# Kernel tuning notes

Hardware: AMD Instinct MI355X
Metric: run time of the kernel (lower is better)

## Reference

```python
import jax, jax.numpy as jnp
import numpy as np

K = 4

def grid_sample_bilinear_zeros(img, grid):
    # img: [b,c,H,W]; grid: [b,h,w,2] normalized coords (x,y) in [-1,1]
    # PyTorch grid_sample, mode='bilinear', padding_mode='zeros', align_corners=False
    b, c, H, W = img.shape
    h, w = grid.shape[1], grid.shape[2]
    ix = (grid[..., 0] + 1.0) * (W * 0.5) - 0.5
    iy = (grid[..., 1] + 1.0) * (H * 0.5) - 0.5
    x0 = jnp.floor(ix); y0 = jnp.floor(iy)
    wx1 = ix - x0; wx0 = 1.0 - wx1
    wy1 = iy - y0; wy0 = 1.0 - wy1
    x0i = x0.astype(jnp.int32); y0i = y0.astype(jnp.int32)
    x1i = x0i + 1; y1i = y0i + 1
    imgf = img.reshape(b, c, H * W)
    N = h * w

    def gather(xi, yi, wgt):
        valid = (xi >= 0) & (xi < W) & (yi >= 0) & (yi < H)
        xc = jnp.clip(xi, 0, W - 1); yc = jnp.clip(yi, 0, H - 1)
        idx = (yc * W + xc).reshape(b, 1, N)
        g = jnp.take_along_axis(imgf, jnp.broadcast_to(idx, (b, c, N)), axis=2)
        wv = (wgt * valid.astype(img.dtype)).reshape(b, 1, N)
        return g * wv

    out = (gather(x0i, y0i, wx0 * wy0) + gather(x1i, y0i, wx1 * wy0) +
           gather(x0i, y1i, wx0 * wy1) + gather(x1i, y1i, wx1 * wy1))
    return out.reshape(b, c, h, w)


def setup_inputs() -> dict:
    key = jax.random.key(0)
    ks = jax.random.split(key, 8)
    b, c, h, w = 8, 256, 96, 96
    out_ch = 256
    x = jax.random.normal(ks[0], (b, c, h, w), dtype=jnp.float32)
    Wc = jax.random.normal(ks[1], (out_ch, c), dtype=jnp.float32) * 0.02
    bc = jax.random.normal(ks[2], (out_ch,), dtype=jnp.float32) * 0.02
    Woff = jax.random.normal(ks[3], (K, 2, c), dtype=jnp.float32) * 0.02
    boff = jax.random.normal(ks[4], (K, 2), dtype=jnp.float32) * 0.02
    Wwt = jax.random.normal(ks[5], (K, c), dtype=jnp.float32) * 0.02
    bwt = jax.random.normal(ks[6], (K,), dtype=jnp.float32) * 0.02
    return {"x": x, "Wc": Wc, "bc": bc, "Woff": Woff, "boff": boff, "Wwt": Wwt, "bwt": bwt}


def reference(x, Wc, bc, Woff, boff, Wwt, bwt):
    b, c, h, w = x.shape
    # 1x1 conv projection
    proj = jnp.einsum('bchw,oc->bohw', x, Wc) + bc[None, :, None, None]
    # k flow fields, each [b,2,h,w] -> [k,b,h,w,2]
    flows = jnp.einsum('bchw,koc->kbohw', x, Woff) + boff[:, None, :, None, None]
    flows = jnp.transpose(flows, (0, 1, 3, 4, 2))
    # softmax sampling weights [b,k,h,w]
    logits = jnp.einsum('bchw,kc->bkhw', x, Wwt) + bwt[None, :, None, None]
    weights = jax.nn.softmax(logits, axis=1)
    # base pixel grid (x,y)
    gy, gx = jnp.meshgrid(jnp.arange(h, dtype=x.dtype), jnp.arange(w, dtype=x.dtype), indexing='ij')
    base = jnp.stack((gx, gy), axis=-1)  # [h,w,2]
    vgrid = base[None, None] + flows  # [k,b,h,w,2]
    vx = 2.0 * vgrid[..., 0] / max(w - 1, 1) - 1.0
    vy = 2.0 * vgrid[..., 1] / max(h - 1, 1) - 1.0
    vgrid_scaled = jnp.stack((vx, vy), axis=-1)  # [k,b,h,w,2]
    feats = jax.vmap(lambda g: grid_sample_bilinear_zeros(proj, g))(vgrid_scaled)  # [k,b,o,h,w]
    out = jnp.einsum('kbohw,bkhw->bohw', feats, weights)
    return out
```

## Files before the change

kernel.cpp:

```cpp
#include <hip/hip_runtime.h>

#define HW   9216
#define IMG  96
#define NB   8
#define NK   4

typedef __bf16 bf16x8 __attribute__((ext_vector_type(8)));
typedef float  f32x4  __attribute__((ext_vector_type(4)));

__device__ __forceinline__ unsigned short f2bf(float f) {
    unsigned int u = __float_as_uint(f);
    u += 0x7FFFu + ((u >> 16) & 1u);
    return (unsigned short)(u >> 16);
}

extern "C" __global__ __launch_bounds__(256, 4)
void prep_kernel(const float* __restrict__ x,
                 const float* __restrict__ Wc,
                 const float* __restrict__ Woff,
                 const float* __restrict__ boff,
                 const float* __restrict__ Wwt,
                 const float* __restrict__ bwt,
                 unsigned short* __restrict__ xbt,
                 unsigned short* __restrict__ Wcb,
                 float2* __restrict__ coords,
                 float* __restrict__ wts)
{
    __shared__ __align__(16) unsigned short tile[64 * 266];

    const int t   = threadIdx.x;
    const int bxr = blockIdx.x;

    if (bxr >= NB * 144) {
        int u = ((bxr - NB * 144) * 256 + t) * 4;
        float4 v = *(const float4*)(Wc + u);
        union { unsigned short h[4]; int2 p; } pk;
        pk.h[0] = f2bf(v.x); pk.h[1] = f2bf(v.y);
        pk.h[2] = f2bf(v.z); pk.h[3] = f2bf(v.w);
        *(int2*)(Wcb + u) = pk.p;
        return;
    }

    const int b  = bxr / 144;
    const int p0 = (bxr % 144) * 64;
    const int px = t & 63;
    const int g  = __builtin_amdgcn_readfirstlane(t >> 6);

    float acc[12];
    #pragma unroll
    for (int j = 0; j < 12; ++j) acc[j] = 0.f;

    const float* xb = x + ((size_t)(b * 256 + g * 64)) * HW + p0 + px;
    unsigned int* trow = (unsigned int*)tile;

    for (int i0 = 0; i0 < 64; i0 += 8) {
        float v[8];
        #pragma unroll
        for (int q = 0; q < 8; ++q)
            v[q] = xb[(size_t)(i0 + q) * HW];
        #pragma unroll
        for (int q = 0; q < 8; ++q) {
            const int c = g * 64 + i0 + q;
            #pragma unroll
            for (int j = 0; j < 8; ++j) acc[j] += v[q] * Woff[j * 256 + c];
            #pragma unroll
            for (int j = 0; j < 4; ++j) acc[8 + j] += v[q] * Wwt[j * 256 + c];
        }
        #pragma unroll
        for (int q = 0; q < 8; q += 2) {
            unsigned int pk = (unsigned int)f2bf(v[q]) | ((unsigned int)f2bf(v[q + 1]) << 16);
            trow[px * 133 + ((g * 64 + i0 + q) >> 1)] = pk;
        }
    }

    __syncthreads();
    #pragma unroll
    for (int r = 0; r < 8; ++r) {
        int u = t + 256 * r;
        int sub = u & 31, p2 = u >> 5;
        int4 v = *(const int4*)(tile + p2 * 266 + sub * 8);
        *(int4*)(xbt + ((size_t)b * HW + p0 + p2) * 256 + sub * 8) = v;
    }
    __syncthreads();

    float* red = (float*)tile;
    #pragma unroll
    for (int j = 0; j < 12; ++j)
        red[(g * 64 + px) * 12 + j] = acc[j];
    __syncthreads();

    if (t < 64) {
        float s[12];
        #pragma unroll
        for (int j = 0; j < 12; ++j)
            s[j] = red[(0 * 64 + px) * 12 + j] + red[(1 * 64 + px) * 12 + j] +
                   red[(2 * 64 + px) * 12 + j] + red[(3 * 64 + px) * 12 + j];

        const int p = p0 + px;
        const float pyf = (float)(p / IMG);
        const float pxf = (float)(p % IMG);

        #pragma unroll
        for (int k = 0; k < NK; ++k) {
            float fx = s[k * 2 + 0] + boff[k * 2 + 0];
            float fy = s[k * 2 + 1] + boff[k * 2 + 1];
            float vx = 2.0f * (pxf + fx) / 95.0f - 1.0f;
            float vy = 2.0f * (pyf + fy) / 95.0f - 1.0f;
            float ix = (vx + 1.0f) * 48.0f - 0.5f;
            float iy = (vy + 1.0f) * 48.0f - 0.5f;
            coords[((size_t)k * NB + b) * HW + p] = make_float2(ix, iy);
        }
        float l0 = s[8] + bwt[0], l1 = s[9] + bwt[1];
        float l2 = s[10] + bwt[2], l3 = s[11] + bwt[3];
        float m = fmaxf(fmaxf(l0, l1), fmaxf(l2, l3));
        float e0 = __expf(l0 - m), e1 = __expf(l1 - m);
        float e2 = __expf(l2 - m), e3 = __expf(l3 - m);
        float inv = 1.0f / (e0 + e1 + e2 + e3);
        wts[((size_t)0 * NB + b) * HW + p] = e0 * inv;
        wts[((size_t)1 * NB + b) * HW + p] = e1 * inv;
        wts[((size_t)2 * NB + b) * HW + p] = e2 * inv;
        wts[((size_t)3 * NB + b) * HW + p] = e3 * inv;
    }
}

extern "C" __global__ __launch_bounds__(256, 3)
void fused_kernel(const unsigned short* __restrict__ Wcb,
                  const unsigned short* __restrict__ xbt,
                  const float2* __restrict__ coords,
                  const float* __restrict__ wts,
                  const float* __restrict__ bc,
                  float* __restrict__ out)
{
    __shared__ __align__(16) unsigned char lds[49408];
    unsigned short* BsU   = (unsigned short*)lds;
    unsigned short* AsU   = (unsigned short*)(lds + 32768);
    float*          cw    = (float*)(lds + 32768);
    unsigned int*   ci    = (unsigned int*)(lds + 36864);
    float*          wsumL = (float*)(lds + 49152);

    const int t  = threadIdx.x;
    const int bx = blockIdx.x;
    const int b  = bx & 7;
    const int p0 = (bx >> 3) * 64;

    {
        const int px = t & 63;
        const int k  = t >> 6;
        const int p  = p0 + px;
        float2 cc = coords[((size_t)k * NB + b) * HW + p];
        float wk  = wts[((size_t)k * NB + b) * HW + p];
        float x0f = floorf(cc.x), y0f = floorf(cc.y);
        float wx1 = cc.x - x0f, wx0 = 1.0f - wx1;
        float wy1 = cc.y - y0f, wy0 = 1.0f - wy1;
        int x0 = (int)x0f, y0 = (int)y0f;
        int x1 = x0 + 1,   y1 = y0 + 1;
        float vx0 = (x0 >= 0 && x0 < IMG) ? 1.f : 0.f;
        float vx1 = (x1 >= 0 && x1 < IMG) ? 1.f : 0.f;
        float vy0 = (y0 >= 0 && y0 < IMG) ? 1.f : 0.f;
        float vy1 = (y1 >= 0 && y1 < IMG) ? 1.f : 0.f;
        int cx0 = min(max(x0, 0), IMG - 1), cx1 = min(max(x1, 0), IMG - 1);
        int cy0 = min(max(y0, 0), IMG - 1), cy1 = min(max(y1, 0), IMG - 1);
        int i0 = cy0 * IMG + cx0, i1 = cy0 * IMG + cx1;
        int i2 = cy1 * IMG + cx0, i3 = cy1 * IMG + cx1;
        float w0 = wk * wx0 * wy0 * vx0 * vy0;
        float w1 = wk * wx1 * wy0 * vx1 * vy0;
        float w2 = wk * wx0 * wy1 * vx0 * vy1;
        float w3 = wk * wx1 * wy1 * vx1 * vy1;
        *(float4*)(cw + px * 16 + k * 4) = make_float4(w0, w1, w2, w3);
        uint2 ip;
        ip.x = (unsigned int)i0 | ((unsigned int)i1 << 16);
        ip.y = (unsigned int)i2 | ((unsigned int)i3 << 16);
        *(uint2*)(ci + px * 8 + k * 2) = ip;
    }
    __syncthreads();

    {
        if (t < 64) {
            float s = 0.f;
            #pragma unroll
            for (int j = 0; j < 16; ++j) s += cw[t * 16 + j];
            wsumL[t] = s;
        }
        const int pxl = t >> 5, ch = t & 31;
        const unsigned short* gbase = xbt + (size_t)b * HW * 256 + ch * 8;
        #pragma unroll 2
        for (int rep = 0; rep < 8; ++rep) {
            const int px = rep * 8 + pxl;
            float wl[16];
            #pragma unroll
            for (int q = 0; q < 4; ++q) {
                float4 wv = *(const float4*)(cw + px * 16 + q * 4);
                wl[q * 4 + 0] = wv.x; wl[q * 4 + 1] = wv.y;
                wl[q * 4 + 2] = wv.z; wl[q * 4 + 3] = wv.w;
            }
            unsigned int ip[8];
            #pragma unroll
            for (int q = 0; q < 2; ++q) {
                uint4 iv = *(const uint4*)(ci + px * 8 + q * 4);
                ip[q * 4 + 0] = iv.x; ip[q * 4 + 1] = iv.y;
                ip[q * 4 + 2] = iv.z; ip[q * 4 + 3] = iv.w;
            }
            int4 v[16];
            #pragma unroll
            for (int j = 0; j < 16; ++j) {
                unsigned int idx = (ip[j >> 1] >> ((j & 1) * 16)) & 0xFFFFu;
                v[j] = *(const int4*)(gbase + (size_t)idx * 256);
            }
            float acc[8];
            #pragma unroll
            for (int i = 0; i < 8; ++i) acc[i] = 0.f;
            #pragma unroll
            for (int j = 0; j < 16; ++j) {
                const unsigned int* u = (const unsigned int*)&v[j];
                float wj = wl[j];
                #pragma unroll
                for (int q = 0; q < 4; ++q) {
                    float lo = __uint_as_float(u[q] << 16);
                    float hi = __uint_as_float(u[q] & 0xFFFF0000u);
                    acc[2 * q + 0] += wj * lo;
                    acc[2 * q + 1] += wj * hi;
                }
            }
            union { unsigned short h[8]; int4 v4; } pk;
            #pragma unroll
            for (int i = 0; i < 8; ++i) pk.h[i] = f2bf(acc[i]);
            const int pos = ch ^ (px & 7);
            *(int4*)(BsU + px * 256 + pos * 8) = pk.v4;
        }
    }
    __syncthreads();

    const int lane = t & 63, wave = t >> 6;
    const int wm = wave * 64;
    const int l15 = lane & 15, quad = lane >> 4;

    f32x4 acc[4][4];
    #pragma unroll
    for (int mt = 0; mt < 4; ++mt)
        #pragma unroll
        for (int nt = 0; nt < 4; ++nt)
            acc[mt][nt] = (f32x4){0.f, 0.f, 0.f, 0.f};

    for (int k0 = 0; k0 < 256; k0 += 32) {
        #pragma unroll
        for (int i = 0; i < 4; ++i) {
            int u = t + 256 * i;
            int row = u >> 2, sub = u & 3;
            int sub_g = sub ^ ((row >> 1) & 3);
            __builtin_amdgcn_global_load_lds(
                (const __attribute__((address_space(1))) void*)(Wcb + (size_t)row * 256 + k0 + sub_g * 8),
                (__attribute__((address_space(3))) void*)(AsU + u * 8), 16, 0, 0);
        }
        __syncthreads();
        bf16x8 af[4], bf[4];
        #pragma unroll
        for (int mt = 0; mt < 4; ++mt) {
            int row = wm + mt * 16 + l15;
            int pos = quad ^ ((row >> 1) & 3);
            af[mt] = *(const bf16x8*)(const void*)(AsU + row * 32 + pos * 8);
        }
        #pragma unroll
        for (int nt = 0; nt < 4; ++nt) {
            int row = nt * 16 + l15;
            int pos = ((k0 >> 3) + quad) ^ (row & 7);
            bf[nt] = *(const bf16x8*)(const void*)(BsU + row * 256 + pos * 8);
        }
        #pragma unroll
        for (int mt = 0; mt < 4; ++mt)
            #pragma unroll
            for (int nt = 0; nt < 4; ++nt)
                acc[mt][nt] = __builtin_amdgcn_mfma_f32_16x16x32_bf16(af[mt], bf[nt], acc[mt][nt], 0, 0, 0);
        __syncthreads();
    }

    float wv[4];
    #pragma unroll
    for (int nt = 0; nt < 4; ++nt)
        wv[nt] = wsumL[nt * 16 + l15];

    #pragma unroll
    for (int mt = 0; mt < 4; ++mt) {
        int ob = wm + mt * 16 + quad * 4;
        #pragma unroll
        for (int reg = 0; reg < 4; ++reg) {
            int o = ob + reg;
            float bias = bc[o];
            float* dst = out + ((size_t)b * 256 + o) * HW + p0 + l15;
            #pragma unroll
            for (int nt = 0; nt < 4; ++nt)
                dst[nt * 16] = acc[mt][nt][reg] + bias * wv[nt];
        }
    }
}

extern "C" void kernel_launch(void* const* d_in, const int* in_sizes, int n_in,
                              void* d_out, int out_size, void* d_ws, size_t ws_size,
                              hipStream_t stream)
{
    const float* x    = (const float*)d_in[0];
    const float* Wc   = (const float*)d_in[1];
    const float* bc   = (const float*)d_in[2];
    const float* Woff = (const float*)d_in[3];
    const float* boff = (const float*)d_in[4];
    const float* Wwt  = (const float*)d_in[5];
    const float* bwt  = (const float*)d_in[6];
    float* out = (float*)d_out;

    char* ws = (char*)d_ws;
    unsigned short* xbt  = (unsigned short*)(ws);
    float2* coords       = (float2*)(ws + 75497472);
    float*  wts          = (float*)(ws + 77856768);
    unsigned short* Wcb  = (unsigned short*)(ws + 79036416);

    prep_kernel<<<dim3(NB * 144 + 64), dim3(256), 0, stream>>>(
        x, Wc, Woff, boff, Wwt, bwt, xbt, Wcb, coords, wts);
    fused_kernel<<<dim3(NB * 144), dim3(256), 0, stream>>>(
        Wcb, xbt, coords, wts, bc, out);
}
```

Before: 189.6 us.

## Load GEMM A fragments from global with register prefetch; widen prep blocks

The fused kernel no longer stages the bf16 weight tile through LDS with global_load_lds and two barriers per k-step. Each wave now reads its own A fragments straight from global memory (the weights are small and likely cached) and prefetches the next k-slice into registers. This drops the per-iteration syncs, shrinks LDS use and raises the occupancy hint to 4 blocks per CU. Separately, the prep kernel moves to 512-thread blocks, each wave handling 32 channels, with an 8-way reduction; its aggressive launch bound hint may constrain registers.

```diff
diff --git a/kernel.cpp b/kernel.cpp
--- a/kernel.cpp
+++ b/kernel.cpp
@@ -14,7 +14,7 @@
     return (unsigned short)(u >> 16);
 }
 
-extern "C" __global__ __launch_bounds__(256, 4)
+extern "C" __global__ __launch_bounds__(512, 8)
 void prep_kernel(const float* __restrict__ x,
                  const float* __restrict__ Wc,
                  const float* __restrict__ Woff,
@@ -32,7 +32,7 @@
     const int bxr = blockIdx.x;
 
     if (bxr >= NB * 144) {
-        int u = ((bxr - NB * 144) * 256 + t) * 4;
+        int u = ((bxr - NB * 144) * 512 + t) * 4;
         float4 v = *(const float4*)(Wc + u);
         union { unsigned short h[4]; int2 p; } pk;
         pk.h[0] = f2bf(v.x); pk.h[1] = f2bf(v.y);
@@ -50,17 +50,17 @@
     #pragma unroll
     for (int j = 0; j < 12; ++j) acc[j] = 0.f;
 
-    const float* xb = x + ((size_t)(b * 256 + g * 64)) * HW + p0 + px;
+    const float* xb = x + ((size_t)(b * 256 + g * 32)) * HW + p0 + px;
     unsigned int* trow = (unsigned int*)tile;
 
-    for (int i0 = 0; i0 < 64; i0 += 8) {
+    for (int i0 = 0; i0 < 32; i0 += 8) {
         float v[8];
         #pragma unroll
         for (int q = 0; q < 8; ++q)
             v[q] = xb[(size_t)(i0 + q) * HW];
         #pragma unroll
         for (int q = 0; q < 8; ++q) {
-            const int c = g * 64 + i0 + q;
+            const int c = g * 32 + i0 + q;
             #pragma unroll
             for (int j = 0; j < 8; ++j) acc[j] += v[q] * Woff[j * 256 + c];
             #pragma unroll
@@ -69,14 +69,14 @@
         #pragma unroll
         for (int q = 0; q < 8; q += 2) {
             unsigned int pk = (unsigned int)f2bf(v[q]) | ((unsigned int)f2bf(v[q + 1]) << 16);
-            trow[px * 133 + ((g * 64 + i0 + q) >> 1)] = pk;
-        }
-    }
-
-    __syncthreads();
-    #pragma unroll
-    for (int r = 0; r < 8; ++r) {
-        int u = t + 256 * r;
+            trow[px * 133 + ((g * 32 + i0 + q) >> 1)] = pk;
+        }
+    }
+
+    __syncthreads();
+    #pragma unroll
+    for (int r = 0; r < 4; ++r) {
+        int u = t + 512 * r;
         int sub = u & 31, p2 = u >> 5;
         int4 v = *(const int4*)(tile + p2 * 266 + sub * 8);
         *(int4*)(xbt + ((size_t)b * HW + p0 + p2) * 256 + sub * 8) = v;
@@ -92,9 +92,13 @@
     if (t < 64) {
         float s[12];
         #pragma unroll
-        for (int j = 0; j < 12; ++j)
-            s[j] = red[(0 * 64 + px) * 12 + j] + red[(1 * 64 + px) * 12 + j] +
-                   red[(2 * 64 + px) * 12 + j] + red[(3 * 64 + px) * 12 + j];
+        for (int j = 0; j < 12; ++j) {
+            float sj = 0.f;
+            #pragma unroll
+            for (int w = 0; w < 8; ++w)
+                sj += red[(w * 64 + px) * 12 + j];
+            s[j] = sj;
+        }
 
         const int p = p0 + px;
         const float pyf = (float)(p / IMG);
@@ -123,7 +127,7 @@
     }
 }
 
-extern "C" __global__ __launch_bounds__(256, 3)
+extern "C" __global__ __launch_bounds__(256, 4)
 void fused_kernel(const unsigned short* __restrict__ Wcb,
                   const unsigned short* __restrict__ xbt,
                   const float2* __restrict__ coords,
@@ -131,12 +135,11 @@
                   const float* __restrict__ bc,
                   float* __restrict__ out)
 {
-    __shared__ __align__(16) unsigned char lds[49408];
+    __shared__ __align__(16) unsigned char lds[39168];
     unsigned short* BsU   = (unsigned short*)lds;
-    unsigned short* AsU   = (unsigned short*)(lds + 32768);
     float*          cw    = (float*)(lds + 32768);
     unsigned int*   ci    = (unsigned int*)(lds + 36864);
-    float*          wsumL = (float*)(lds + 49152);
+    float*          wsumL = (float*)(lds + 38912);
 
     const int t  = threadIdx.x;
     const int bx = blockIdx.x;
@@ -241,24 +244,26 @@
         for (int nt = 0; nt < 4; ++nt)
             acc[mt][nt] = (f32x4){0.f, 0.f, 0.f, 0.f};
 
+    const unsigned short* aRow0 = Wcb + (size_t)(wm +  0 + l15) * 256 + quad * 8;
+    const unsigned short* aRow1 = Wcb + (size_t)(wm + 16 + l15) * 256 + quad * 8;
+    const unsigned short* aRow2 = Wcb + (size_t)(wm + 32 + l15) * 256 + quad * 8;
+    const unsigned short* aRow3 = Wcb + (size_t)(wm + 48 + l15) * 256 + quad * 8;
+
+    bf16x8 af[4];
+    af[0] = *(const bf16x8*)(const void*)(aRow0);
+    af[1] = *(const bf16x8*)(const void*)(aRow1);
+    af[2] = *(const bf16x8*)(const void*)(aRow2);
+    af[3] = *(const bf16x8*)(const void*)(aRow3);
+
     for (int k0 = 0; k0 < 256; k0 += 32) {
-        #pragma unroll
-        for (int i = 0; i < 4; ++i) {
-            int u = t + 256 * i;
-            int row = u >> 2, sub = u & 3;
-            int sub_g = sub ^ ((row >> 1) & 3);
-            __builtin_amdgcn_global_load_lds(
-                (const __attribute__((address_space(1))) void*)(Wcb + (size_t)row * 256 + k0 + sub_g * 8),
-                (__attribute__((address_space(3))) void*)(AsU + u * 8), 16, 0, 0);
-        }
-        __syncthreads();
-        bf16x8 af[4], bf[4];
-        #pragma unroll
-        for (int mt = 0; mt < 4; ++mt) {
-            int row = wm + mt * 16 + l15;
-            int pos = quad ^ ((row >> 1) & 3);
-            af[mt] = *(const bf16x8*)(const void*)(AsU + row * 32 + pos * 8);
-        }
+        bf16x8 afn[4];
+        if (k0 + 32 < 256) {
+            afn[0] = *(const bf16x8*)(const void*)(aRow0 + k0 + 32);
+            afn[1] = *(const bf16x8*)(const void*)(aRow1 + k0 + 32);
+            afn[2] = *(const bf16x8*)(const void*)(aRow2 + k0 + 32);
+            afn[3] = *(const bf16x8*)(const void*)(aRow3 + k0 + 32);
+        }
+        bf16x8 bf[4];
         #pragma unroll
         for (int nt = 0; nt < 4; ++nt) {
             int row = nt * 16 + l15;
@@ -270,7 +275,8 @@
             #pragma unroll
             for (int nt = 0; nt < 4; ++nt)
                 acc[mt][nt] = __builtin_amdgcn_mfma_f32_16x16x32_bf16(af[mt], bf[nt], acc[mt][nt], 0, 0, 0);
-        __syncthreads();
+        #pragma unroll
+        for (int mt = 0; mt < 4; ++mt) af[mt] = afn[mt];
     }
 
     float wv[4];
@@ -312,7 +318,7 @@
     float*  wts          = (float*)(ws + 77856768);
     unsigned short* Wcb  = (unsigned short*)(ws + 79036416);
 
-    prep_kernel<<<dim3(NB * 144 + 64), dim3(256), 0, stream>>>(
+    prep_kernel<<<dim3(NB * 144 + 32), dim3(512), 0, stream>>>(
         x, Wc, Woff, boff, Wwt, bwt, xbt, Wcb, coords, wts);
     fused_kernel<<<dim3(NB * 144), dim3(256), 0, stream>>>(
         Wcb, xbt, coords, wts, bc, out);
```

Measured after the change: 207.2 us. 9.3% more time.
